# Performance work log

Hardware: AMD Instinct MI355X
Metric: run time of the kernel (lower is better)

The kernel has to match this reference:

```python
import jax, jax.numpy as jnp
import numpy as np

LATENT_DIM = 32
INPUT_DIM = 16
N_UNITS = 20
N_TRAJ = 4096
T = 512


def setup_inputs() -> dict:
    key = jax.random.key(0)
    ks = jax.random.split(key, 8)
    cat_dim = LATENT_DIM + INPUT_DIM
    s1 = 1.0 / np.sqrt(cat_dim)
    s2 = 1.0 / np.sqrt(N_UNITS)
    return {
        "data": jax.random.normal(ks[0], (N_TRAJ, T, INPUT_DIM), dtype=jnp.float32),
        "time_steps": jnp.arange(T, dtype=jnp.float32),
        "Wu1": jax.random.normal(ks[1], (cat_dim, N_UNITS), dtype=jnp.float32) * s1,
        "bu1": jnp.zeros((N_UNITS,), dtype=jnp.float32),
        "Wu2": jax.random.normal(ks[2], (N_UNITS, LATENT_DIM), dtype=jnp.float32) * s2,
        "bu2": jnp.zeros((LATENT_DIM,), dtype=jnp.float32),
        "Wr1": jax.random.normal(ks[3], (cat_dim, N_UNITS), dtype=jnp.float32) * s1,
        "br1": jnp.zeros((N_UNITS,), dtype=jnp.float32),
        "Wr2": jax.random.normal(ks[4], (N_UNITS, LATENT_DIM), dtype=jnp.float32) * s2,
        "br2": jnp.zeros((LATENT_DIM,), dtype=jnp.float32),
        "Wn1": jax.random.normal(ks[5], (cat_dim, N_UNITS), dtype=jnp.float32) * s1,
        "bn1": jnp.zeros((N_UNITS,), dtype=jnp.float32),
        "Wn2": jax.random.normal(ks[6], (N_UNITS, LATENT_DIM), dtype=jnp.float32) * s2,
        "bn2": jnp.zeros((LATENT_DIM,), dtype=jnp.float32),
    }


def _mlp(h, W1, b1, W2, b2):
    # 2-layer MLP with tanh hidden, linear out
    return jnp.tanh(h @ W1 + b1) @ W2 + b2


def reference(data, time_steps, Wu1, bu1, Wu2, bu2, Wr1, br1, Wr2, br2, Wn1, bn1, Wn2, bn2):
    n_traj = data.shape[0]
    latent_dim = Wu2.shape[1]

    def step(prev_y, xi):
        yc = jnp.concatenate([prev_y, xi], axis=-1)            # [B, L+D]
        u = jax.nn.sigmoid(_mlp(yc, Wu1, bu1, Wu2, bu2))       # update gate
        r = jax.nn.sigmoid(_mlp(yc, Wr1, br1, Wr2, br2))       # reset gate
        cc = jnp.concatenate([prev_y * r, xi], axis=-1)
        n = jnp.tanh(_mlp(cc, Wn1, bn1, Wn2, bn2))             # candidate state
        new_y = (1.0 - u) * n + u * prev_y
        return new_y, new_y

    prev_y = jnp.zeros((n_traj, latent_dim), dtype=data.dtype)
    xs = jnp.swapaxes(data, 0, 1)                              # [T, B, D]
    yi, ys = jax.lax.scan(step, prev_y, xs)
    latent_ys = jnp.swapaxes(ys, 0, 1)                         # [B, T, L]
    return yi, latent_ys
```

## Files before the change

kernel.cpp:

```cpp
#include <hip/hip_runtime.h>

#define T_STEPS 512
#define NTRAJ   4096
#define LAT     32
#define INPD    16
#define HID     20
#define CAT     48

__device__ __forceinline__ float fast_tanh(float x) {
    float e = __expf(2.0f * x);
    float r = __builtin_amdgcn_rcpf(e + 1.0f);
    return fmaf(-2.0f, r, 1.0f);
}
__device__ __forceinline__ float fast_sigmoid(float x) {
    float e = __expf(-x);
    return __builtin_amdgcn_rcpf(e + 1.0f);
}

__global__ __launch_bounds__(256) void rnn_fused(
    const float* __restrict__ data,
    const float* __restrict__ Wu1, const float* __restrict__ bu1,
    const float* __restrict__ Wu2, const float* __restrict__ bu2,
    const float* __restrict__ Wr1, const float* __restrict__ br1,
    const float* __restrict__ Wr2, const float* __restrict__ br2,
    const float* __restrict__ Wn1, const float* __restrict__ bn1,
    const float* __restrict__ Wn2, const float* __restrict__ bn2,
    float* __restrict__ out_yi, float* __restrict__ out_lat)
{
    __shared__ __align__(16) float YC[4][CAT];
    __shared__ __align__(16) float CCb[4][CAT];
    __shared__ __align__(16) float H1[4][64];
    __shared__ __align__(16) float HN[4][32];

    const int tid  = threadIdx.x;
    const int w    = tid >> 6;
    const int lane = tid & 63;
    const int c    = lane & 31;
    const int g    = lane >> 5;
    const int b    = (blockIdx.x << 2) + w;

    float* yc = YC[w];
    float* cc = CCb[w];
    float* h1 = H1[w];
    float* hn = HN[w];

    float wa[CAT], wb[HID], wc[24], wd[12];
    float ba, bb, bc, bd;
    {
        const float* W1 = g ? Wr1 : Wu1;
        const float* B1 = g ? br1 : bu1;
        const float* W2 = g ? Wr2 : Wu2;
        const float* B2 = g ? br2 : bu2;
        const bool real = (c < HID);
        #pragma unroll
        for (int k = 0; k < CAT; ++k) {
            int idx = real ? (k * HID + c) : 0;
            wa[k] = real ? W1[idx] : 0.0f;
        }
        ba = real ? B1[c] : 0.0f;
        #pragma unroll
        for (int k = 0; k < HID; ++k) wb[k] = W2[k * LAT + c];
        bb = B2[c];
        #pragma unroll
        for (int k = 0; k < 24; ++k) {
            int idx = real ? ((g * 24 + k) * HID + c) : 0;
            wc[k] = real ? Wn1[idx] : 0.0f;
        }
        bc = (real && g == 0) ? bn1[c] : 0.0f;
        #pragma unroll
        for (int k = 0; k < 12; ++k) {
            int row = g * 12 + k;
            int idx = (row < HID) ? (row * LAT + c) : 0;
            wd[k] = (row < HID) ? Wn2[idx] : 0.0f;
        }
        bd = (g == 0) ? bn2[c] : 0.0f;
    }

    const size_t xbase = (size_t)b * T_STEPS * INPD + (lane & 15);
    float xc = data[xbase];
    float xn = data[xbase + INPD];

    float y_reg = 0.0f;
    float u_reg = 0.0f;

    for (int t = 0; t < T_STEPS; ++t) {
        if (lane < 32) {
            yc[c] = y_reg;
            if (lane < 16) { yc[32 + lane] = xc; cc[32 + lane] = xc; }
        }
        int tf = t + 2; tf = (tf < T_STEPS) ? tf : (T_STEPS - 1);
        float xf = data[xbase + (size_t)tf * INPD];

        asm volatile("s_waitcnt lgkmcnt(0)" ::: "memory");

        float a0 = ba, a1 = 0.0f;
        #pragma unroll
        for (int kk = 0; kk < 12; ++kk) {
            float4 v = *(const float4*)(yc + kk * 4);
            a0 = fmaf(v.x, wa[kk*4+0], a0);
            a1 = fmaf(v.y, wa[kk*4+1], a1);
            a0 = fmaf(v.z, wa[kk*4+2], a0);
            a1 = fmaf(v.w, wa[kk*4+3], a1);
        }
        h1[lane] = fast_tanh(a0 + a1);
        asm volatile("s_waitcnt lgkmcnt(0)" ::: "memory");

        a0 = bb; a1 = 0.0f;
        const float* hsrc = h1 + g * 32;
        #pragma unroll
        for (int kk = 0; kk < 5; ++kk) {
            float4 v = *(const float4*)(hsrc + kk * 4);
            a0 = fmaf(v.x, wb[kk*4+0], a0);
            a1 = fmaf(v.y, wb[kk*4+1], a1);
            a0 = fmaf(v.z, wb[kk*4+2], a0);
            a1 = fmaf(v.w, wb[kk*4+3], a1);
        }
        float gate = fast_sigmoid(a0 + a1);
        if (lane < 32) u_reg = gate;
        float y_other = __shfl_xor(y_reg, 32);
        if (lane >= 32) cc[c] = gate * y_other;
        asm volatile("s_waitcnt lgkmcnt(0)" ::: "memory");

        a0 = bc; a1 = 0.0f;
        #pragma unroll
        for (int kk = 0; kk < 6; ++kk) {
            float4 v = *(const float4*)(cc + g * 24 + kk * 4);
            a0 = fmaf(v.x, wc[kk*4+0], a0);
            a1 = fmaf(v.y, wc[kk*4+1], a1);
            a0 = fmaf(v.z, wc[kk*4+2], a0);
            a1 = fmaf(v.w, wc[kk*4+3], a1);
        }
        float cpart = a0 + a1;
        float csum = cpart + __shfl_xor(cpart, 32);
        if (lane < 32) hn[c] = fast_tanh(csum);
        asm volatile("s_waitcnt lgkmcnt(0)" ::: "memory");

        a0 = bd; a1 = 0.0f;
        #pragma unroll
        for (int kk = 0; kk < 3; ++kk) {
            float4 v = *(const float4*)(hn + g * 12 + kk * 4);
            a0 = fmaf(v.x, wd[kk*4+0], a0);
            a1 = fmaf(v.y, wd[kk*4+1], a1);
            a0 = fmaf(v.z, wd[kk*4+2], a0);
            a1 = fmaf(v.w, wd[kk*4+3], a1);
        }
        float npart = a0 + a1;
        float nsum = npart + __shfl_xor(npart, 32);
        float n = fast_tanh(nsum);
        if (lane < 32) {
            float ny = fmaf(u_reg, y_reg - n, n);
            out_lat[((size_t)b * T_STEPS + t) * LAT + c] = ny;
            y_reg = ny;
        }
        xc = xn; xn = xf;
    }

    if (lane < 32) out_yi[(size_t)b * LAT + c] = y_reg;
}

extern "C" void kernel_launch(void* const* d_in, const int* in_sizes, int n_in,
                              void* d_out, int out_size, void* d_ws, size_t ws_size,
                              hipStream_t stream) {
    const float* data = (const float*)d_in[0];
    const float* Wu1 = (const float*)d_in[2];
    const float* bu1 = (const float*)d_in[3];
    const float* Wu2 = (const float*)d_in[4];
    const float* bu2 = (const float*)d_in[5];
    const float* Wr1 = (const float*)d_in[6];
    const float* br1 = (const float*)d_in[7];
    const float* Wr2 = (const float*)d_in[8];
    const float* br2 = (const float*)d_in[9];
    const float* Wn1 = (const float*)d_in[10];
    const float* bn1 = (const float*)d_in[11];
    const float* Wn2 = (const float*)d_in[12];
    const float* bn2 = (const float*)d_in[13];

    float* out_yi  = (float*)d_out;
    float* out_lat = out_yi + (size_t)NTRAJ * LAT;

    rnn_fused<<<NTRAJ / 4, 256, 0, stream>>>(
        data, Wu1, bu1, Wu2, bu2, Wr1, br1, Wr2, br2, Wn1, bn1, Wn2, bn2,
        out_yi, out_lat);
}
```

Baseline: 948.6 us.

## Replace LDS staging in GRU step with cross-lane shuffles

Removes the per-wave shared-memory buffers and the explicit lgkmcnt waits. All four matrix-vector products in each recurrent step now broadcast operands with `__shfl` instead of float4 LDS reads. The candidate-state output layer is now computed in full by both wave halves rather than split in two and combined with a shuffle. This trades a few wide LDS reads for many per-element shuffles, which may compile to ds_bpermute and could add LDS-path traffic and latency on the serial critical path.

Result: slower. 2.434 ms (+156.6%).

```diff
diff --git a/kernel.cpp b/kernel.cpp
--- a/kernel.cpp
+++ b/kernel.cpp
@@ -27,11 +27,6 @@
     const float* __restrict__ Wn2, const float* __restrict__ bn2,
     float* __restrict__ out_yi, float* __restrict__ out_lat)
 {
-    __shared__ __align__(16) float YC[4][CAT];
-    __shared__ __align__(16) float CCb[4][CAT];
-    __shared__ __align__(16) float H1[4][64];
-    __shared__ __align__(16) float HN[4][32];
-
     const int tid  = threadIdx.x;
     const int w    = tid >> 6;
     const int lane = tid & 63;
@@ -39,12 +34,7 @@
     const int g    = lane >> 5;
     const int b    = (blockIdx.x << 2) + w;
 
-    float* yc = YC[w];
-    float* cc = CCb[w];
-    float* h1 = H1[w];
-    float* hn = HN[w];
-
-    float wa[CAT], wb[HID], wc[24], wd[12];
+    float wa[CAT], wb[HID], wc[24], wd[HID];
     float ba, bb, bc, bd;
     {
         const float* W1 = g ? Wr1 : Wu1;
@@ -62,100 +52,85 @@
         for (int k = 0; k < HID; ++k) wb[k] = W2[k * LAT + c];
         bb = B2[c];
         #pragma unroll
-        for (int k = 0; k < 24; ++k) {
-            int idx = real ? ((g * 24 + k) * HID + c) : 0;
-            wc[k] = real ? Wn1[idx] : 0.0f;
+        for (int kk = 0; kk < 24; ++kk) {
+            int idx = real ? ((g * 24 + kk) * HID + c) : 0;
+            wc[kk] = real ? Wn1[idx] : 0.0f;
         }
         bc = (real && g == 0) ? bn1[c] : 0.0f;
         #pragma unroll
-        for (int k = 0; k < 12; ++k) {
-            int row = g * 12 + k;
-            int idx = (row < HID) ? (row * LAT + c) : 0;
-            wd[k] = (row < HID) ? Wn2[idx] : 0.0f;
-        }
-        bd = (g == 0) ? bn2[c] : 0.0f;
+        for (int k = 0; k < HID; ++k) wd[k] = Wn2[k * LAT + c];
+        bd = bn2[c];
     }
 
-    const size_t xbase = (size_t)b * T_STEPS * INPD + (lane & 15);
-    float xc = data[xbase];
-    float xn = data[xbase + INPD];
+    const float* xptr = data + (size_t)b * T_STEPS * INPD + (lane & 15);
+    float x0 = xptr[0];
+    float x1 = xptr[INPD];
 
-    float y_reg = 0.0f;
-    float u_reg = 0.0f;
+    float y = 0.0f;
+    float* olat = out_lat + (size_t)b * T_STEPS * LAT + c;
+
+    const int bsrc = lane & 32;
+    const int csrc = g * 24;
 
     for (int t = 0; t < T_STEPS; ++t) {
-        if (lane < 32) {
-            yc[c] = y_reg;
-            if (lane < 16) { yc[32 + lane] = xc; cc[32 + lane] = xc; }
+        int tf = t + 2; tf = (tf < T_STEPS) ? tf : (T_STEPS - 1);
+        float x2 = xptr[(size_t)tf * INPD];
+
+        float pool = (lane < 32) ? y : x0;
+        float a0 = ba, a1 = 0.0f, a2 = 0.0f, a3 = 0.0f;
+        #pragma unroll
+        for (int k = 0; k < CAT; k += 4) {
+            a0 = fmaf(__shfl(pool, k + 0), wa[k + 0], a0);
+            a1 = fmaf(__shfl(pool, k + 1), wa[k + 1], a1);
+            a2 = fmaf(__shfl(pool, k + 2), wa[k + 2], a2);
+            a3 = fmaf(__shfl(pool, k + 3), wa[k + 3], a3);
         }
-        int tf = t + 2; tf = (tf < T_STEPS) ? tf : (T_STEPS - 1);
-        float xf = data[xbase + (size_t)tf * INPD];
+        float h1 = fast_tanh((a0 + a1) + (a2 + a3));
 
-        asm volatile("s_waitcnt lgkmcnt(0)" ::: "memory");
+        float b0 = bb, b1 = 0.0f, b2 = 0.0f, b3 = 0.0f;
+        #pragma unroll
+        for (int k = 0; k < HID; k += 4) {
+            b0 = fmaf(__shfl(h1, bsrc + k + 0), wb[k + 0], b0);
+            b1 = fmaf(__shfl(h1, bsrc + k + 1), wb[k + 1], b1);
+            b2 = fmaf(__shfl(h1, bsrc + k + 2), wb[k + 2], b2);
+            b3 = fmaf(__shfl(h1, bsrc + k + 3), wb[k + 3], b3);
+        }
+        float gate = fast_sigmoid((b0 + b1) + (b2 + b3));
 
-        float a0 = ba, a1 = 0.0f;
+        float rb  = __shfl(gate, 32 + c);
+        float ccv = rb * y;
+        float pol2 = (lane < 32) ? ccv : x0;
+
+        float c0 = bc, c1 = 0.0f, c2 = 0.0f, c3 = 0.0f;
         #pragma unroll
-        for (int kk = 0; kk < 12; ++kk) {
-            float4 v = *(const float4*)(yc + kk * 4);
-            a0 = fmaf(v.x, wa[kk*4+0], a0);
-            a1 = fmaf(v.y, wa[kk*4+1], a1);
-            a0 = fmaf(v.z, wa[kk*4+2], a0);
-            a1 = fmaf(v.w, wa[kk*4+3], a1);
+        for (int kk = 0; kk < 24; kk += 4) {
+            c0 = fmaf(__shfl(pol2, csrc + kk + 0), wc[kk + 0], c0);
+            c1 = fmaf(__shfl(pol2, csrc + kk + 1), wc[kk + 1], c1);
+            c2 = fmaf(__shfl(pol2, csrc + kk + 2), wc[kk + 2], c2);
+            c3 = fmaf(__shfl(pol2, csrc + kk + 3), wc[kk + 3], c3);
         }
-        h1[lane] = fast_tanh(a0 + a1);
-        asm volatile("s_waitcnt lgkmcnt(0)" ::: "memory");
+        float cp = (c0 + c1) + (c2 + c3);
+        float cs = cp + __shfl_xor(cp, 32);
+        float hn = fast_tanh(cs);
 
-        a0 = bb; a1 = 0.0f;
-        const float* hsrc = h1 + g * 32;
+        float d0 = bd, d1 = 0.0f, d2 = 0.0f, d3 = 0.0f;
         #pragma unroll
-        for (int kk = 0; kk < 5; ++kk) {
-            float4 v = *(const float4*)(hsrc + kk * 4);
-            a0 = fmaf(v.x, wb[kk*4+0], a0);
-            a1 = fmaf(v.y, wb[kk*4+1], a1);
-            a0 = fmaf(v.z, wb[kk*4+2], a0);
-            a1 = fmaf(v.w, wb[kk*4+3], a1);
+        for (int k = 0; k < HID; k += 4) {
+            d0 = fmaf(__shfl(hn, k + 0), wd[k + 0], d0);
+            d1 = fmaf(__shfl(hn, k + 1), wd[k + 1], d1);
+            d2 = fmaf(__shfl(hn, k + 2), wd[k + 2], d2);
+            d3 = fmaf(__shfl(hn, k + 3), wd[k + 3], d3);
         }
-        float gate = fast_sigmoid(a0 + a1);
-        if (lane < 32) u_reg = gate;
-        float y_other = __shfl_xor(y_reg, 32);
-        if (lane >= 32) cc[c] = gate * y_other;
-        asm volatile("s_waitcnt lgkmcnt(0)" ::: "memory");
+        float n = fast_tanh((d0 + d1) + (d2 + d3));
 
-        a0 = bc; a1 = 0.0f;
-        #pragma unroll
-        for (int kk = 0; kk < 6; ++kk) {
-            float4 v = *(const float4*)(cc + g * 24 + kk * 4);
-            a0 = fmaf(v.x, wc[kk*4+0], a0);
-            a1 = fmaf(v.y, wc[kk*4+1], a1);
-            a0 = fmaf(v.z, wc[kk*4+2], a0);
-            a1 = fmaf(v.w, wc[kk*4+3], a1);
-        }
-        float cpart = a0 + a1;
-        float csum = cpart + __shfl_xor(cpart, 32);
-        if (lane < 32) hn[c] = fast_tanh(csum);
-        asm volatile("s_waitcnt lgkmcnt(0)" ::: "memory");
+        float ny = fmaf(gate, y - n, n);
+        y = ny;
+        if (lane < 32) olat[(size_t)t * LAT] = ny;
 
-        a0 = bd; a1 = 0.0f;
-        #pragma unroll
-        for (int kk = 0; kk < 3; ++kk) {
-            float4 v = *(const float4*)(hn + g * 12 + kk * 4);
-            a0 = fmaf(v.x, wd[kk*4+0], a0);
-            a1 = fmaf(v.y, wd[kk*4+1], a1);
-            a0 = fmaf(v.z, wd[kk*4+2], a0);
-            a1 = fmaf(v.w, wd[kk*4+3], a1);
-        }
-        float npart = a0 + a1;
-        float nsum = npart + __shfl_xor(npart, 32);
-        float n = fast_tanh(nsum);
-        if (lane < 32) {
-            float ny = fmaf(u_reg, y_reg - n, n);
-            out_lat[((size_t)b * T_STEPS + t) * LAT + c] = ny;
-            y_reg = ny;
-        }
-        xc = xn; xn = xf;
+        x0 = x1; x1 = x2;
     }
 
-    if (lane < 32) out_yi[(size_t)b * LAT + c] = y_reg;
+    if (lane < 32) out_yi[(size_t)b * LAT + c] = y;
 }
 
 extern "C" void kernel_launch(void* const* d_in, const int* in_sizes, int n_in,
```
